# Optimization experiments

Measured on AMD Instinct MI355X. Metric: run time of the kernel, lower is better.

## Reference

```python
import jax, jax.numpy as jnp
import numpy as np

B, S, HID = 2, 1024, 4096
NH, NKV = 32, 8            # query heads, kv heads (GQA)
D = HID // NH              # head_size = 128
G = NH // NKV              # groups = 4
SCALE = D ** -0.5


def setup_inputs() -> dict:
    key = jax.random.key(0)
    k1, k2, k3 = jax.random.split(key, 3)
    hidden_states = jax.random.normal(k1, (B, S, HID), dtype=jnp.float32)
    # rotary tables: dim=head_size, base=10000 (PositionRotaryEmbedding.static)
    inv_freq = 1.0 / (10000.0 ** (jnp.arange(0, D, 2, dtype=jnp.float32) / D))  # [D/2]
    t = jnp.arange(S, dtype=jnp.float32)
    freqs = jnp.outer(t, inv_freq)                       # [S, D/2]
    cos, sin = jnp.cos(freqs), jnp.sin(freqs)
    wqkv = jax.random.normal(k2, (HID, (NH + 2 * NKV) * D), dtype=jnp.float32) * (HID ** -0.5)
    wo = jax.random.normal(k3, (NH * D, HID), dtype=jnp.float32) * (HID ** -0.5)
    return {"hidden_states": hidden_states, "cos": cos, "sin": sin, "wqkv": wqkv, "wo": wo}


def _rope(x, cos, sin):
    # interleaved-pair rotary (TGI convention); x: [B,S,H,D], cos/sin: [S,D/2]
    x1, x2 = x[..., 0::2], x[..., 1::2]
    c = cos[None, :, None, :]
    s = sin[None, :, None, :]
    r1 = x1 * c - x2 * s
    r2 = x1 * s + x2 * c
    return jnp.stack([r1, r2], axis=-1).reshape(x.shape)


def reference(hidden_states, cos, sin, wqkv, wo):
    qkv = hidden_states @ wqkv                                  # [B,S,(NH+2*NKV)*D]
    q = qkv[..., : NH * D].reshape(B, S, NH, D)
    k = qkv[..., NH * D : (NH + NKV) * D].reshape(B, S, NKV, D)
    v = qkv[..., (NH + NKV) * D :].reshape(B, S, NKV, D)
    q = _rope(q, cos, sin)
    k = _rope(k, cos, sin)
    # GQA: group query heads over kv heads
    qg = q.reshape(B, S, NKV, G, D)
    scores = jnp.einsum('bqkgd,bskd->bkgqs', qg, k) * SCALE     # [B,NKV,G,S,S]
    causal = jnp.tril(jnp.ones((S, S), dtype=bool))
    scores = jnp.where(causal, scores, jnp.finfo(scores.dtype).min)
    p = jax.nn.softmax(scores, axis=-1)
    out = jnp.einsum('bkgqs,bskd->bqkgd', p, v).reshape(B, S, NH * D)
    return out @ wo                                             # [B,S,HID]
```

## Files before the change

kernel.cpp:

```cpp
#include <hip/hip_runtime.h>
#include <hip/hip_bf16.h>

typedef __bf16 bf16;
typedef __attribute__((ext_vector_type(2))) __bf16 bf16x2;
typedef __attribute__((ext_vector_type(4))) __bf16 bf16x4;
typedef __attribute__((ext_vector_type(8))) __bf16 bf16x8;
typedef __attribute__((ext_vector_type(4))) float f32x4;

#define NB 2
#define SEQ 1024
#define HIDN 4096
#define NH 32
#define NKV 8
#define DH 128
#define QKV_N 6144
static constexpr float SCALE = 0.08838834764831845f;

#define MFMA(a, b, c) __builtin_amdgcn_mfma_f32_16x16x32_bf16((a), (b), (c), 0, 0, 0)

__device__ __forceinline__ void async16(const void* g, void* l) {
  __builtin_amdgcn_global_load_lds(
      (const __attribute__((address_space(1))) unsigned int*)g,
      (__attribute__((address_space(3))) unsigned int*)l,
      16, 0, 0);
}

__device__ __forceinline__ void barrier_raw() {
  asm volatile("" ::: "memory");
  __builtin_amdgcn_s_barrier();
  asm volatile("" ::: "memory");
}
#define VMCNT(n) asm volatile("s_waitcnt vmcnt(" #n ")" ::: "memory")
#define LGKM0 asm volatile("s_waitcnt lgkmcnt(0)" ::: "memory")

__global__ __launch_bounds__(256) void cvt_f32_bf16(const float* __restrict__ src,
                                                    bf16* __restrict__ dst, int n4) {
  int i = blockIdx.x * 256 + threadIdx.x;
  if (i >= n4) return;
  const float4 v = ((const float4*)src)[i];
  bf16x4 o = {(bf16)v.x, (bf16)v.y, (bf16)v.z, (bf16)v.w};
  ((bf16x4*)dst)[i] = o;
}

__global__ __launch_bounds__(256) void transpose_cvt(const float* __restrict__ src,
                                                     bf16* __restrict__ dst, int R, int C) {
  __shared__ float tl[64][65];
  const int i0 = blockIdx.y * 64, j0 = blockIdx.x * 64;
  const int r = threadIdx.x >> 2, c = (threadIdx.x & 3) * 16;
  const float* S = src + (size_t)(i0 + r) * C + j0 + c;
#pragma unroll
  for (int e = 0; e < 4; ++e) *(float4*)&tl[r][c + e * 4] = *(const float4*)&S[e * 4];
  __syncthreads();
  bf16x8 o0, o1;
#pragma unroll
  for (int e = 0; e < 8; ++e) {
    o0[e] = (bf16)tl[c + e][r];
    o1[e] = (bf16)tl[c + 8 + e][r];
  }
  bf16* D = dst + (size_t)(j0 + r) * R + i0 + c;
  *(bf16x8*)&D[0] = o0;
  *(bf16x8*)&D[8] = o1;
}

__global__ __launch_bounds__(256) void vtrans(const bf16* __restrict__ src,
                                              bf16* __restrict__ dst) {
  __shared__ bf16 tl[64][72];
  const int bk = blockIdx.z;
  const int s0 = blockIdx.x * 64, d0 = blockIdx.y * 64;
  const bf16* S = src + ((size_t)bk * SEQ + s0) * DH + d0;
  bf16* D = dst + ((size_t)bk * DH + d0) * SEQ + s0;
  const int r = threadIdx.x >> 2, c = (threadIdx.x & 3) * 16;
  *(bf16x8*)&tl[r][c] = *(const bf16x8*)&S[(size_t)r * DH + c];
  *(bf16x8*)&tl[r][c + 8] = *(const bf16x8*)&S[(size_t)r * DH + c + 8];
  __syncthreads();
  bf16x8 o0, o1;
#pragma unroll
  for (int e = 0; e < 8; ++e) {
    o0[e] = tl[c + e][r];
    o1[e] = tl[c + 8 + e][r];
  }
  *(bf16x8*)&D[(size_t)r * SEQ + c] = o0;
  *(bf16x8*)&D[(size_t)r * SEQ + c + 8] = o1;
}

template <int BN, int MODE>
__global__ __launch_bounds__(512, 2) void gemm_dp(const bf16* __restrict__ A,
                                                  const bf16* __restrict__ BT,
                                                  void* __restrict__ Cout,
                                                  int N, int K,
                                                  const float* __restrict__ cosp,
                                                  const float* __restrict__ sinp,
                                                  bf16* __restrict__ Qo,
                                                  bf16* __restrict__ Ko,
                                                  bf16* __restrict__ Vo) {
  extern __shared__ char smem[];
  constexpr int CA = 128 * 64 * 2;
  constexpr int CB = BN * 64 * 2;
  constexpr int BUF = CA + CB;
  constexpr int UNITS = BUF / 8192;
  constexpr int FN = BN / 64;
  const int t = threadIdx.x, lane = t & 63, w = t >> 6;
  const int l16 = lane & 15, lq = lane >> 4;
  const int wm = w >> 2, wn = w & 3;

  const int nwg = gridDim.x;
  const int lin = ((int)blockIdx.x & 7) * (nwg >> 3) + ((int)blockIdx.x >> 3);
  const int m0 = (lin & 15) * 128;
  const int n0 = (lin >> 4) * BN;

  const int srow = t >> 3;
  const int sslot = (t & 7) ^ (srow & 7);
  const bf16* gsrc[UNITS];
  gsrc[0] = A + (size_t)(m0 + srow) * K + sslot * 8;
  gsrc[1] = A + (size_t)(m0 + 64 + srow) * K + sslot * 8;
#pragma unroll
  for (int u = 2; u < UNITS; ++u)
    gsrc[u] = BT + (size_t)(n0 + (u - 2) * 64 + srow) * K + sslot * 8;

  int aoff[4], boff[FN];
#pragma unroll
  for (int f = 0; f < 4; ++f) {
    const int r = wm * 64 + f * 16 + l16;
    aoff[f] = r * 128 + ((lq ^ (r & 7)) << 4);
  }
#pragma unroll
  for (int j = 0; j < FN; ++j) {
    const int r = wn * (BN / 4) + j * 16 + l16;
    boff[j] = CA + r * 128 + ((lq ^ (r & 7)) << 4);
  }

  auto stage = [&](int kt) {
    char* d = smem + (kt & 1) * BUF + t * 16;
#pragma unroll
    for (int u = 0; u < UNITS; ++u) async16(gsrc[u] + (size_t)kt * 64, d + u * 8192);
  };

  f32x4 acc[4][FN] = {};
  const int NT = K >> 6;

  stage(0);

  for (int kt = 0; kt < NT; ++kt) {
    const char* buf = smem + (kt & 1) * BUF;
    barrier_raw();
    if (kt + 1 < NT) {
      stage(kt + 1);
      if constexpr (UNITS == 8) { VMCNT(8); } else { VMCNT(6); }
    } else {
      VMCNT(0);
    }
#pragma unroll
    for (int kk = 0; kk < 2; ++kk) {
      const int kx = kk * 64;
      bf16x8 af[4], bfr[FN];
#pragma unroll
      for (int f = 0; f < 4; ++f) af[f] = *(const bf16x8*)(buf + (aoff[f] ^ kx));
#pragma unroll
      for (int j = 0; j < FN; ++j) bfr[j] = *(const bf16x8*)(buf + (boff[j] ^ kx));
      __builtin_amdgcn_s_setprio(1);
#pragma unroll
      for (int f = 0; f < 4; ++f)
#pragma unroll
        for (int j = 0; j < FN; ++j) acc[f][j] = MFMA(af[f], bfr[j], acc[f][j]);
      __builtin_amdgcn_s_setprio(0);
    }
    LGKM0;
  }

  if constexpr (MODE == 2) {
    barrier_raw();
    float* csl = (float*)smem;
    float* snl = (float*)(smem + 32768);
    const int s0 = m0 & 1023;
    const f32x4* cs = (const f32x4*)(cosp + s0 * 64);
    const f32x4* sn = (const f32x4*)(sinp + s0 * 64);
#pragma unroll
    for (int i = 0; i < 4; ++i) {
      ((f32x4*)csl)[t + i * 512] = cs[t + i * 512];
      ((f32x4*)snl)[t + i * 512] = sn[t + i * 512];
    }
    barrier_raw();
#pragma unroll
    for (int f = 0; f < 4; ++f)
#pragma unroll
      for (int j = 0; j < FN; ++j)
#pragma unroll
        for (int r = 0; r < 4; ++r) {
          const int row = m0 + wm * 64 + f * 16 + lq * 4 + r;
          const int col = n0 + wn * (BN / 4) + j * 16 + l16;
          const float v = acc[f][j][r];
          const float part = __shfl_xor(v, 1);
          const int bb = row >> 10, s = row & 1023;
          const int srel = wm * 64 + f * 16 + lq * 4 + r;
          if (col < 4096) {
            const int h = col >> 7, d = col & 127;
            const float c = csl[srel * 64 + (d >> 1)];
            const float sv = snl[srel * 64 + (d >> 1)];
            const float o = (l16 & 1) ? (part * sv + v * c) : (v * c - part * sv);
            Qo[((size_t)(bb * NH + h) * SEQ + s) * DH + d] = (bf16)(o * SCALE);
          } else if (col < 5120) {
            const int idx = col - 4096, kvh = idx >> 7, d = idx & 127;
            const float c = csl[srel * 64 + (d >> 1)];
            const float sv = snl[srel * 64 + (d >> 1)];
            const float o = (l16 & 1) ? (part * sv + v * c) : (v * c - part * sv);
            Ko[((size_t)(bb * NKV + kvh) * SEQ + s) * DH + d] = (bf16)o;
          } else {
            const int idx = col - 5120, kvh = idx >> 7, d = idx & 127;
            Vo[((size_t)(bb * NKV + kvh) * SEQ + s) * DH + d] = (bf16)v;
          }
        }
  } else {
#pragma unroll
    for (int f = 0; f < 4; ++f)
#pragma unroll
      for (int j = 0; j < FN; ++j)
#pragma unroll
        for (int r = 0; r < 4; ++r) {
          const int row = m0 + wm * 64 + f * 16 + lq * 4 + r;
          const int col = n0 + wn * (BN / 4) + j * 16 + l16;
          if (MODE == 1)
            ((bf16*)Cout)[(size_t)row * N + col] = (bf16)acc[f][j][r];
          else
            ((float*)Cout)[(size_t)row * N + col] = acc[f][j][r];
        }
  }
}

__global__ __launch_bounds__(512, 2) void flash_attn(const bf16* __restrict__ Q,
                                                     const bf16* __restrict__ K,
                                                     const bf16* __restrict__ VT,
                                                     bf16* __restrict__ O) {
  extern __shared__ char smem[];
  const int t = threadIdx.x, lane = t & 63, w = t >> 6;
  const int l16 = lane & 15, lq = lane >> 4;
  const int p = blockIdx.x;
  const int b = p >> 7, h = (p >> 2) & 31, Tb = p & 3;
  const int kvh = h >> 2;

  const bf16* Qb = Q + (size_t)(b * NH + h) * SEQ * DH;
  const bf16* Kb = K + (size_t)(b * NKV + kvh) * SEQ * DH;
  const bf16* Vb = VT + (size_t)(b * NKV + kvh) * DH * SEQ;

  const int qrA = Tb * 128 + w * 16;
  const int qrB = (7 - Tb) * 128 + w * 16;
  const int nAw = (qrA >> 6) + 1;
  const int nBw = (qrB >> 6) + 1;
  const int NT = 16 - 2 * Tb;

  bf16* plw = (bf16*)(smem + 98304) + w * (2 * 16 * 72);

  const bf16* kSrc = Kb + (size_t)(t >> 4) * DH + 8 * ((t & 15) ^ ((t >> 4) & 7));
  const bf16* vSrc = Vb + (size_t)(t >> 3) * SEQ + 8 * ((t & 7) ^ ((t >> 3) & 7));

  auto stage = [&](int kv) {
    char* bufb = smem + (kv % 3) * 32768;
    async16(kSrc + (size_t)(kv * 64) * DH, bufb + t * 16);
    async16(kSrc + (size_t)(kv * 64 + 32) * DH, bufb + 8192 + t * 16);
    async16(vSrc + kv * 64, bufb + 16384 + t * 16);
    async16(vSrc + (size_t)64 * SEQ + kv * 64, bufb + 24576 + t * 16);
  };

  int KX[4], VX[2];
#pragma unroll
  for (int kk = 0; kk < 4; ++kk) KX[kk] = ((kk * 4 + lq) ^ (l16 & 7)) << 4;
#pragma unroll
  for (int c = 0; c < 2; ++c) VX[c] = ((c * 4 + lq) ^ (l16 & 7)) << 4;

  bf16x8 qfA[4], qfB[4];
#pragma unroll
  for (int kk = 0; kk < 4; ++kk) {
    qfA[kk] = *(const bf16x8*)&Qb[(size_t)(qrA + l16) * DH + kk * 32 + lq * 8];
    qfB[kk] = *(const bf16x8*)&Qb[(size_t)(qrB + l16) * DH + kk * 32 + lq * 8];
  }

  f32x4 accA[8] = {}, accB[8] = {};
  float mA[4], lA[4], mB[4], lB[4];
#pragma unroll
  for (int r = 0; r < 4; ++r) {
    mA[r] = mB[r] = -INFINITY;
    lA[r] = lB[r] = 0.f;
  }

  auto finish = [&](f32x4(&s)[4], float(&m)[4], float(&l)[4], f32x4(&acc)[8], int slot,
                    bool mask, int kv, int qr) {
    if (mask) {
#pragma unroll
      for (int nt = 0; nt < 4; ++nt)
#pragma unroll
        for (int r = 0; r < 4; ++r)
          if (kv * 64 + nt * 16 + l16 > qr + lq * 4 + r) s[nt][r] = -INFINITY;
    }
#pragma unroll
    for (int r = 0; r < 4; ++r) {
      float mx = fmaxf(fmaxf(s[0][r], s[1][r]), fmaxf(s[2][r], s[3][r]));
#pragma unroll
      for (int off = 1; off < 16; off <<= 1) mx = fmaxf(mx, __shfl_xor(mx, off));
      const float mn = fmaxf(m[r], mx);
      const float corr = __expf(m[r] - mn);
      m[r] = mn;
      float ps = 0.f;
#pragma unroll
      for (int nt = 0; nt < 4; ++nt) {
        const float pv = __expf(s[nt][r] - mn);
        s[nt][r] = pv;
        ps += pv;
      }
#pragma unroll
      for (int off = 1; off < 16; off <<= 1) ps += __shfl_xor(ps, off);
      l[r] = l[r] * corr + ps;
#pragma unroll
      for (int j = 0; j < 8; ++j) acc[j][r] *= corr;
    }
#pragma unroll
    for (int nt = 0; nt < 4; ++nt)
#pragma unroll
      for (int r = 0; r < 4; ++r)
        plw[slot * 1152 + (lq * 4 + r) * 72 + nt * 16 + l16] = (bf16)s[nt][r];
  };

  stage(0);
  stage(1);
  VMCNT(4);
  barrier_raw();

  for (int kv = 0; kv < NT; ++kv) {
    const char* kbuf = smem + (kv % 3) * 32768;
    const char* vbuf = kbuf + 16384;
    if (kv + 2 < NT) stage(kv + 2);

    if (kv < nAw) {
      f32x4 sA[4] = {}, sB[4] = {};
      __builtin_amdgcn_s_setprio(1);
#pragma unroll
      for (int nt = 0; nt < 4; ++nt) {
        const char* kr = kbuf + (nt * 16 + l16) * 256;
        bf16x8 k0 = *(const bf16x8*)(kr + KX[0]);
        bf16x8 k1 = *(const bf16x8*)(kr + KX[1]);
        bf16x8 k2 = *(const bf16x8*)(kr + KX[2]);
        bf16x8 k3 = *(const bf16x8*)(kr + KX[3]);
        sA[nt] = MFMA(qfA[0], k0, sA[nt]);
        sB[nt] = MFMA(qfB[0], k0, sB[nt]);
        sA[nt] = MFMA(qfA[1], k1, sA[nt]);
        sB[nt] = MFMA(qfB[1], k1, sB[nt]);
        sA[nt] = MFMA(qfA[2], k2, sA[nt]);
        sB[nt] = MFMA(qfB[2], k2, sB[nt]);
        sA[nt] = MFMA(qfA[3], k3, sA[nt]);
        sB[nt] = MFMA(qfB[3], k3, sB[nt]);
      }
      __builtin_amdgcn_s_setprio(0);
      finish(sA, mA, lA, accA, 0, kv == nAw - 1, kv, qrA);
      finish(sB, mB, lB, accB, 1, kv == nBw - 1, kv, qrB);
      bf16x8 pA0 = *(const bf16x8*)&plw[l16 * 72 + lq * 8];
      bf16x8 pA1 = *(const bf16x8*)&plw[l16 * 72 + 32 + lq * 8];
      bf16x8 pB0 = *(const bf16x8*)&plw[1152 + l16 * 72 + lq * 8];
      bf16x8 pB1 = *(const bf16x8*)&plw[1152 + l16 * 72 + 32 + lq * 8];
      __builtin_amdgcn_s_setprio(1);
#pragma unroll
      for (int j = 0; j < 8; ++j) {
        const char* vr = vbuf + (j * 16 + l16) * 128;
        bf16x8 v0 = *(const bf16x8*)(vr + VX[0]);
        bf16x8 v1 = *(const bf16x8*)(vr + VX[1]);
        accA[j] = MFMA(pA0, v0, accA[j]);
        accB[j] = MFMA(pB0, v0, accB[j]);
        accA[j] = MFMA(pA1, v1, accA[j]);
        accB[j] = MFMA(pB1, v1, accB[j]);
      }
      __builtin_amdgcn_s_setprio(0);
    } else if (kv < nBw) {
      f32x4 sB[4] = {};
      __builtin_amdgcn_s_setprio(1);
#pragma unroll
      for (int nt = 0; nt < 4; ++nt) {
        const char* kr = kbuf + (nt * 16 + l16) * 256;
        bf16x8 k0 = *(const bf16x8*)(kr + KX[0]);
        bf16x8 k1 = *(const bf16x8*)(kr + KX[1]);
        bf16x8 k2 = *(const bf16x8*)(kr + KX[2]);
        bf16x8 k3 = *(const bf16x8*)(kr + KX[3]);
        sB[nt] = MFMA(qfB[0], k0, sB[nt]);
        sB[nt] = MFMA(qfB[1], k1, sB[nt]);
        sB[nt] = MFMA(qfB[2], k2, sB[nt]);
        sB[nt] = MFMA(qfB[3], k3, sB[nt]);
      }
      __builtin_amdgcn_s_setprio(0);
      finish(sB, mB, lB, accB, 1, kv == nBw - 1, kv, qrB);
      bf16x8 pB0 = *(const bf16x8*)&plw[1152 + l16 * 72 + lq * 8];
      bf16x8 pB1 = *(const bf16x8*)&plw[1152 + l16 * 72 + 32 + lq * 8];
      __builtin_amdgcn_s_setprio(1);
#pragma unroll
      for (int j = 0; j < 8; ++j) {
        const char* vr = vbuf + (j * 16 + l16) * 128;
        bf16x8 v0 = *(const bf16x8*)(vr + VX[0]);
        bf16x8 v1 = *(const bf16x8*)(vr + VX[1]);
        accB[j] = MFMA(pB0, v0, accB[j]);
        accB[j] = MFMA(pB1, v1, accB[j]);
      }
      __builtin_amdgcn_s_setprio(0);
    }

    if (kv + 2 < NT) { VMCNT(4); } else { VMCNT(0); }
    barrier_raw();
  }

  auto wout = [&](f32x4(&acc)[8], float(&l)[4], int qr) {
#pragma unroll
    for (int r = 0; r < 4; ++r) {
      const float inv = 1.f / l[r];
      const size_t orow = ((size_t)b * SEQ + qr + lq * 4 + r) * HIDN + h * DH;
#pragma unroll
      for (int j = 0; j < 8; ++j) O[orow + j * 16 + l16] = (bf16)(acc[j][r] * inv);
    }
  };
  wout(accA, lA, qrA);
  wout(accB, lB, qrB);
}

extern "C" void kernel_launch(void* const* d_in, const int* in_sizes, int n_in,
                              void* d_out, int out_size, void* d_ws, size_t ws_size,
                              hipStream_t stream) {
  const float* hidden = (const float*)d_in[0];
  const float* cosp = (const float*)d_in[1];
  const float* sinp = (const float*)d_in[2];
  const float* wqkv = (const float*)d_in[3];
  const float* wo = (const float*)d_in[4];
  float* out = (float*)d_out;

  char* ws = (char*)d_ws;
  bf16* hiddenB = (bf16*)(ws);
  bf16* wqkvT  = (bf16*)(ws + 16777216);
  bf16* woT    = (bf16*)(ws + 67108864);
  bf16* Vtmp   = (bf16*)(ws + 100663296);
  bf16* Qb     = (bf16*)(ws + 125829120);
  bf16* Kb     = (bf16*)(ws + 142606336);
  bf16* VTb    = (bf16*)(ws + 146800640);
  bf16* attnB  = hiddenB;

  cvt_f32_bf16<<<8192, 256, 0, stream>>>(hidden, hiddenB, 2097152);
  transpose_cvt<<<dim3(96, 64), 256, 0, stream>>>(wqkv, wqkvT, 4096, 6144);
  transpose_cvt<<<dim3(64, 64), 256, 0, stream>>>(wo, woT, 4096, 4096);
  gemm_dp<384, 2><<<dim3(256), 512, 131072, stream>>>(hiddenB, wqkvT, nullptr, 6144, 4096,
                                                      cosp, sinp, Qb, Kb, Vtmp);
  vtrans<<<dim3(16, 2, 16), 256, 0, stream>>>(Vtmp, VTb);
  flash_attn<<<dim3(256), 512, 135168, stream>>>(Qb, Kb, VTb, attnB);
  gemm_dp<256, 0><<<dim3(256), 512, 98304, stream>>>(attnB, woT, out, 4096, 4096,
                                                     nullptr, nullptr, nullptr, nullptr,
                                                     nullptr);
}
```

Before: 286.2 us.

## Triple-buffer GEMM K-loop, unify tile to 128x256, widen weight transpose tiles

The GEMM now uses a three-stage LDS ring with two tiles in flight and a single barrier per iteration, replacing the double-buffered loop. The QKV projection moves from 128x384 tiles on 256 blocks to 128x256 tiles on 384 blocks. The weight transpose kernel switches to 128x64 tiles with 512 threads. The aim is to hide global-load latency better and balance work across CUs, at the cost of 144KB of LDS per block, which likely limits occupancy to one block per CU.

```diff
diff --git a/kernel.cpp b/kernel.cpp
--- a/kernel.cpp
+++ b/kernel.cpp
@@ -42,24 +42,29 @@
   ((bf16x4*)dst)[i] = o;
 }
 
-__global__ __launch_bounds__(256) void transpose_cvt(const float* __restrict__ src,
+__global__ __launch_bounds__(512) void transpose_cvt(const float* __restrict__ src,
                                                      bf16* __restrict__ dst, int R, int C) {
-  __shared__ float tl[64][65];
-  const int i0 = blockIdx.y * 64, j0 = blockIdx.x * 64;
-  const int r = threadIdx.x >> 2, c = (threadIdx.x & 3) * 16;
-  const float* S = src + (size_t)(i0 + r) * C + j0 + c;
-#pragma unroll
-  for (int e = 0; e < 4; ++e) *(float4*)&tl[r][c + e * 4] = *(const float4*)&S[e * 4];
+  __shared__ float tl[128][68];
+  const int j0 = blockIdx.x * 64, i0 = blockIdx.y * 128;
+  {
+    const int r = threadIdx.x >> 2, c = (threadIdx.x & 3) * 16;
+    const float* S = src + (size_t)(i0 + r) * C + j0 + c;
+#pragma unroll
+    for (int e = 0; e < 4; ++e) *(float4*)&tl[r][c + e * 4] = *(const float4*)&S[e * 4];
+  }
   __syncthreads();
-  bf16x8 o0, o1;
-#pragma unroll
-  for (int e = 0; e < 8; ++e) {
-    o0[e] = (bf16)tl[c + e][r];
-    o1[e] = (bf16)tl[c + 8 + e][r];
-  }
-  bf16* D = dst + (size_t)(j0 + r) * R + i0 + c;
-  *(bf16x8*)&D[0] = o0;
-  *(bf16x8*)&D[8] = o1;
+  {
+    const int j = threadIdx.x >> 3, ic = (threadIdx.x & 7) * 16;
+    bf16x8 o0, o1;
+#pragma unroll
+    for (int e = 0; e < 8; ++e) {
+      o0[e] = (bf16)tl[ic + e][j];
+      o1[e] = (bf16)tl[ic + 8 + e][j];
+    }
+    bf16* D = dst + (size_t)(j0 + j) * R + i0 + ic;
+    *(bf16x8*)&D[0] = o0;
+    *(bf16x8*)&D[8] = o1;
+  }
 }
 
 __global__ __launch_bounds__(256) void vtrans(const bf16* __restrict__ src,
@@ -83,7 +88,7 @@
   *(bf16x8*)&D[(size_t)r * SEQ + c + 8] = o1;
 }
 
-template <int BN, int MODE>
+template <int MODE>
 __global__ __launch_bounds__(512, 2) void gemm_dp(const bf16* __restrict__ A,
                                                   const bf16* __restrict__ BT,
                                                   void* __restrict__ Cout,
@@ -95,10 +100,8 @@
                                                   bf16* __restrict__ Vo) {
   extern __shared__ char smem[];
   constexpr int CA = 128 * 64 * 2;
-  constexpr int CB = BN * 64 * 2;
+  constexpr int CB = 256 * 64 * 2;
   constexpr int BUF = CA + CB;
-  constexpr int UNITS = BUF / 8192;
-  constexpr int FN = BN / 64;
   const int t = threadIdx.x, lane = t & 63, w = t >> 6;
   const int l16 = lane & 15, lq = lane >> 4;
   const int wm = w >> 2, wn = w & 3;
@@ -106,69 +109,68 @@
   const int nwg = gridDim.x;
   const int lin = ((int)blockIdx.x & 7) * (nwg >> 3) + ((int)blockIdx.x >> 3);
   const int m0 = (lin & 15) * 128;
-  const int n0 = (lin >> 4) * BN;
+  const int n0 = (lin >> 4) * 256;
 
   const int srow = t >> 3;
   const int sslot = (t & 7) ^ (srow & 7);
-  const bf16* gsrc[UNITS];
+  const bf16* gsrc[6];
   gsrc[0] = A + (size_t)(m0 + srow) * K + sslot * 8;
   gsrc[1] = A + (size_t)(m0 + 64 + srow) * K + sslot * 8;
 #pragma unroll
-  for (int u = 2; u < UNITS; ++u)
+  for (int u = 2; u < 6; ++u)
     gsrc[u] = BT + (size_t)(n0 + (u - 2) * 64 + srow) * K + sslot * 8;
 
-  int aoff[4], boff[FN];
+  int aoff[4], boff[4];
 #pragma unroll
   for (int f = 0; f < 4; ++f) {
-    const int r = wm * 64 + f * 16 + l16;
-    aoff[f] = r * 128 + ((lq ^ (r & 7)) << 4);
-  }
-#pragma unroll
-  for (int j = 0; j < FN; ++j) {
-    const int r = wn * (BN / 4) + j * 16 + l16;
-    boff[j] = CA + r * 128 + ((lq ^ (r & 7)) << 4);
+    const int ra = wm * 64 + f * 16 + l16;
+    aoff[f] = ra * 128 + ((lq ^ (ra & 7)) << 4);
+    const int rb = wn * 64 + f * 16 + l16;
+    boff[f] = CA + rb * 128 + ((lq ^ (rb & 7)) << 4);
   }
 
   auto stage = [&](int kt) {
-    char* d = smem + (kt & 1) * BUF + t * 16;
-#pragma unroll
-    for (int u = 0; u < UNITS; ++u) async16(gsrc[u] + (size_t)kt * 64, d + u * 8192);
+    char* d = smem + (kt % 3) * BUF + t * 16;
+#pragma unroll
+    for (int u = 0; u < 6; ++u) async16(gsrc[u] + (size_t)kt * 64, d + u * 8192);
   };
 
-  f32x4 acc[4][FN] = {};
+  f32x4 acc[4][4] = {};
   const int NT = K >> 6;
 
   stage(0);
+  stage(1);
+  VMCNT(6);
+  barrier_raw();
 
   for (int kt = 0; kt < NT; ++kt) {
-    const char* buf = smem + (kt & 1) * BUF;
-    barrier_raw();
-    if (kt + 1 < NT) {
-      stage(kt + 1);
-      if constexpr (UNITS == 8) { VMCNT(8); } else { VMCNT(6); }
-    } else {
-      VMCNT(0);
-    }
+    const char* buf = smem + (kt % 3) * BUF;
+    if (kt + 2 < NT) stage(kt + 2);
 #pragma unroll
     for (int kk = 0; kk < 2; ++kk) {
       const int kx = kk * 64;
-      bf16x8 af[4], bfr[FN];
+      bf16x8 af[4], bfr[4];
 #pragma unroll
       for (int f = 0; f < 4; ++f) af[f] = *(const bf16x8*)(buf + (aoff[f] ^ kx));
 #pragma unroll
-      for (int j = 0; j < FN; ++j) bfr[j] = *(const bf16x8*)(buf + (boff[j] ^ kx));
+      for (int j = 0; j < 4; ++j) bfr[j] = *(const bf16x8*)(buf + (boff[j] ^ kx));
       __builtin_amdgcn_s_setprio(1);
 #pragma unroll
       for (int f = 0; f < 4; ++f)
 #pragma unroll
-        for (int j = 0; j < FN; ++j) acc[f][j] = MFMA(af[f], bfr[j], acc[f][j]);
+        for (int j = 0; j < 4; ++j) acc[f][j] = MFMA(af[f], bfr[j], acc[f][j]);
       __builtin_amdgcn_s_setprio(0);
     }
+    if (kt + 2 < NT) {
+      VMCNT(6);
+    } else if (kt + 1 < NT) {
+      VMCNT(0);
+    }
     LGKM0;
+    barrier_raw();
   }
 
   if constexpr (MODE == 2) {
-    barrier_raw();
     float* csl = (float*)smem;
     float* snl = (float*)(smem + 32768);
     const int s0 = m0 & 1023;
@@ -183,11 +185,11 @@
 #pragma unroll
     for (int f = 0; f < 4; ++f)
 #pragma unroll
-      for (int j = 0; j < FN; ++j)
+      for (int j = 0; j < 4; ++j)
 #pragma unroll
         for (int r = 0; r < 4; ++r) {
           const int row = m0 + wm * 64 + f * 16 + lq * 4 + r;
-          const int col = n0 + wn * (BN / 4) + j * 16 + l16;
+          const int col = n0 + wn * 64 + j * 16 + l16;
           const float v = acc[f][j][r];
           const float part = __shfl_xor(v, 1);
           const int bb = row >> 10, s = row & 1023;
@@ -213,15 +215,12 @@
 #pragma unroll
     for (int f = 0; f < 4; ++f)
 #pragma unroll
-      for (int j = 0; j < FN; ++j)
+      for (int j = 0; j < 4; ++j)
 #pragma unroll
         for (int r = 0; r < 4; ++r) {
           const int row = m0 + wm * 64 + f * 16 + lq * 4 + r;
-          const int col = n0 + wn * (BN / 4) + j * 16 + l16;
-          if (MODE == 1)
-            ((bf16*)Cout)[(size_t)row * N + col] = (bf16)acc[f][j][r];
-          else
-            ((float*)Cout)[(size_t)row * N + col] = acc[f][j][r];
+          const int col = n0 + wn * 64 + j * 16 + l16;
+          ((float*)Cout)[(size_t)row * N + col] = acc[f][j][r];
         }
   }
 }
@@ -435,13 +434,13 @@
   bf16* attnB  = hiddenB;
 
   cvt_f32_bf16<<<8192, 256, 0, stream>>>(hidden, hiddenB, 2097152);
-  transpose_cvt<<<dim3(96, 64), 256, 0, stream>>>(wqkv, wqkvT, 4096, 6144);
-  transpose_cvt<<<dim3(64, 64), 256, 0, stream>>>(wo, woT, 4096, 4096);
-  gemm_dp<384, 2><<<dim3(256), 512, 131072, stream>>>(hiddenB, wqkvT, nullptr, 6144, 4096,
-                                                      cosp, sinp, Qb, Kb, Vtmp);
+  transpose_cvt<<<dim3(96, 32), 512, 0, stream>>>(wqkv, wqkvT, 4096, 6144);
+  transpose_cvt<<<dim3(64, 32), 512, 0, stream>>>(wo, woT, 4096, 4096);
+  gemm_dp<2><<<dim3(384), 512, 147456, stream>>>(hiddenB, wqkvT, nullptr, 6144, 4096,
+                                                 cosp, sinp, Qb, Kb, Vtmp);
   vtrans<<<dim3(16, 2, 16), 256, 0, stream>>>(Vtmp, VTb);
   flash_attn<<<dim3(256), 512, 135168, stream>>>(Qb, Kb, VTb, attnB);
-  gemm_dp<256, 0><<<dim3(256), 512, 98304, stream>>>(attnB, woT, out, 4096, 4096,
-                                                     nullptr, nullptr, nullptr, nullptr,
-                                                     nullptr);
-}
+  gemm_dp<0><<<dim3(256), 512, 147456, stream>>>(attnB, woT, out, 4096, 4096,
+                                                 nullptr, nullptr, nullptr, nullptr,
+                                                 nullptr);
+}
```

Result: slower. 316.9 us (+10.7%).
